# Kernel optimization log

Hardware: AMD Instinct MI355X
Metric: run time of the kernel (lower is better)

The kernel has to match this reference:

```python
import jax, jax.numpy as jnp
import numpy as np

D = 128          # hidden_dim
R = 16           # num_relations
N = 50000        # num_nodes
E = 800000       # num_edges
P = 256          # number of candidate paths
L = 4            # path length in nodes (max_path_length=3 edges)
NUM_LAYERS = 2


def _layer_norm(x, g, b, eps=1e-5):
    mu = jnp.mean(x, axis=-1, keepdims=True)
    var = jnp.var(x, axis=-1, keepdims=True)
    return (x - mu) * jax.lax.rsqrt(var + eps) * g + b


def _lstm(x, W_ih, W_hh, b):
    # x: (P, L, 2D) -> final hidden state (P, D). PyTorch gate order i,f,g,o.
    h0 = jnp.zeros((x.shape[0], D), x.dtype)
    c0 = jnp.zeros((x.shape[0], D), x.dtype)
    xs = jnp.swapaxes(x, 0, 1)  # (L, P, 2D)

    def step(carry, xt):
        h, c = carry
        gates = xt @ W_ih.T + h @ W_hh.T + b
        i, f, g, o = jnp.split(gates, 4, axis=-1)
        c = jax.nn.sigmoid(f) * c + jax.nn.sigmoid(i) * jnp.tanh(g)
        h = jax.nn.sigmoid(o) * jnp.tanh(c)
        return (h, c), None

    (h, _), _ = jax.lax.scan(step, (h0, c0), xs)
    return h


def setup_inputs() -> dict:
    key = jax.random.key(0)
    ks = jax.random.split(key, 24)
    s = 0.02
    inp = {
        'node_features': jax.random.normal(ks[0], (N, D), jnp.float32),
        'edge_index': jax.random.randint(ks[1], (2, E), 0, N),
        'edge_types': jax.random.randint(ks[2], (E,), 0, R),
        'query_embedding': jax.random.normal(ks[3], (D,), jnp.float32),
        'path_nodes': jax.random.randint(ks[4], (P, L), 0, N),
        'path_relations': jax.random.randint(ks[5], (P, L - 1), 0, R),
        # RGCN params (stacked over layers)
        'W_self': jax.random.normal(ks[6], (NUM_LAYERS, D, D), jnp.float32) * s,
        'b_self': jnp.zeros((NUM_LAYERS, D), jnp.float32),
        'W_rel': jax.random.normal(ks[7], (NUM_LAYERS, R, D, D), jnp.float32) * s,
        'ln_g': jnp.ones((NUM_LAYERS, D), jnp.float32),
        'ln_b': jnp.zeros((NUM_LAYERS, D), jnp.float32),
        # PathEncoder
        'rel_emb': jax.random.normal(ks[8], (R, D), jnp.float32) * s,
        'W_ih_f': jax.random.normal(ks[9], (4 * D, 2 * D), jnp.float32) * s,
        'W_hh_f': jax.random.normal(ks[10], (4 * D, D), jnp.float32) * s,
        'b_f': jnp.zeros((4 * D,), jnp.float32),
        'W_ih_b': jax.random.normal(ks[11], (4 * D, 2 * D), jnp.float32) * s,
        'W_hh_b': jax.random.normal(ks[12], (4 * D, D), jnp.float32) * s,
        'b_b': jnp.zeros((4 * D,), jnp.float32),
        'W_op': jax.random.normal(ks[13], (D, 2 * D), jnp.float32) * s,
        'b_op': jnp.zeros((D,), jnp.float32),
        # similarity scorer
        'W_s1': jax.random.normal(ks[14], (D, 2 * D), jnp.float32) * s,
        'b_s1': jnp.zeros((D,), jnp.float32),
        'W_s2': jax.random.normal(ks[15], (1, D), jnp.float32) * s,
        'b_s2': jnp.zeros((1,), jnp.float32),
    }
    return inp


def reference(node_features, edge_index, edge_types, query_embedding,
              path_nodes, path_relations,
              W_self, b_self, W_rel, ln_g, ln_b,
              rel_emb, W_ih_f, W_hh_f, b_f, W_ih_b, W_hh_b, b_b, W_op, b_op,
              W_s1, b_s1, W_s2, b_s2):
    src, dst = edge_index[0], edge_index[1]
    n = node_features.shape[0]
    deg = jnp.zeros((n,), node_features.dtype).at[dst].add(1.0)
    denom = jnp.maximum(deg, 1.0)[:, None]

    # ---- encode_subgraph: RGCN layers + LayerNorm ----
    x = node_features
    for l in range(NUM_LAYERS):
        trans = jnp.einsum('nd,rdk->rnk', x, W_rel[l])       # (R, N, D)
        msg = trans[edge_types, src]                          # (E, D) gather
        agg = jax.ops.segment_sum(msg, dst, num_segments=n) / denom
        x = jax.nn.relu(x @ W_self[l] + b_self[l] + agg)
        x = _layer_norm(x, ln_g[l], ln_b[l])
    encoded = x

    # ---- PathEncoder, batched over P paths ----
    pn = encoded[path_nodes]                                  # (P, L, D)
    rf = rel_emb[path_relations]                              # (P, L-1, D)
    zero_rel = jnp.zeros((rf.shape[0], 1, D), rf.dtype)
    rf = jnp.concatenate([zero_rel, rf], axis=1)              # (P, L, D)
    seq = jnp.concatenate([pn, rf], axis=-1)                  # (P, L, 2D)

    h_f = _lstm(seq, W_ih_f, W_hh_f, b_f)                     # forward final h
    h_b = _lstm(seq[:, ::-1, :], W_ih_b, W_hh_b, b_b)         # backward final h
    pe = jnp.concatenate([h_f, h_b], axis=-1)                 # (P, 2D)
    pe = jax.nn.relu(pe @ W_op.T + b_op)                      # (P, D)

    # ---- similarity scorer ----
    q = jnp.broadcast_to(query_embedding[None, :], pe.shape)
    comb = jnp.concatenate([pe, q], axis=-1)                  # (P, 2D)
    hdn = jax.nn.relu(comb @ W_s1.T + b_s1)
    sim = jax.nn.sigmoid(hdn @ W_s2.T + b_s2).squeeze(-1)     # (P,)

    return encoded, pe, sim
```

## Files before the change

kernel.cpp:

```cpp
#include <hip/hip_runtime.h>


#define NN 50000
#define EE 800000
#define DD 128
#define RR 16
#define PP 256
#define PADN 50048
#define NSLOT 17
#define CSTRIDE 136

typedef __attribute__((ext_vector_type(4))) float f32x4;
typedef __attribute__((ext_vector_type(2))) float f32x2;
typedef __attribute__((ext_vector_type(8))) short s16x8;

__device__ __forceinline__ float bf2f(unsigned int u16v){
    unsigned int u = u16v << 16;
    return __builtin_bit_cast(float, u);
}
__device__ __forceinline__ unsigned short f2bf(float f){
    unsigned int u = __builtin_bit_cast(unsigned int, f);
    u = u + 0x7fffu + ((u >> 16) & 1u);
    return (unsigned short)(u >> 16);
}

__global__ void k_hist(const int* __restrict__ dst, int* __restrict__ deg,
                       int* __restrict__ rank){
    int e = blockIdx.x*256 + threadIdx.x;
    if (e < EE) rank[e] = atomicAdd(&deg[dst[e]], 1);
}
__global__ void k_scan1(const int* __restrict__ deg, int* __restrict__ bsum){
    __shared__ int sm[256];
    int t = threadIdx.x, i = blockIdx.x*256 + t;
    sm[t] = (i < NN) ? deg[i] : 0;
    __syncthreads();
    for (int o = 128; o > 0; o >>= 1){
        if (t < o) sm[t] += sm[t+o];
        __syncthreads();
    }
    if (t == 0) bsum[blockIdx.x] = sm[0];
}
__global__ void k_scan2(const int* __restrict__ bsum, int* __restrict__ boff){
    __shared__ int sm[256];
    int t = threadIdx.x;
    int v = (t < 196) ? bsum[t] : 0;
    sm[t] = v;
    __syncthreads();
    for (int o = 1; o < 256; o <<= 1){
        int x = (t >= o) ? sm[t-o] : 0;
        __syncthreads();
        sm[t] += x;
        __syncthreads();
    }
    boff[t] = sm[t] - v;
}
__global__ void k_scan3(const int* __restrict__ deg, const int* __restrict__ boff,
                        int* __restrict__ row_start){
    __shared__ int sm[256];
    int t = threadIdx.x, i = blockIdx.x*256 + t;
    int v = (i < NN) ? deg[i] : 0;
    sm[t] = v;
    __syncthreads();
    for (int o = 1; o < 256; o <<= 1){
        int x = (t >= o) ? sm[t-o] : 0;
        __syncthreads();
        sm[t] += x;
        __syncthreads();
    }
    if (i < NN) row_start[i] = boff[blockIdx.x] + sm[t] - v;
    if (i == 0) row_start[NN] = EE;
}
__global__ void k_fill(const int* __restrict__ src, const int* __restrict__ dst,
                       const int* __restrict__ et, const int* __restrict__ row_start,
                       const int* __restrict__ rank, unsigned int* __restrict__ csr){
    int e = blockIdx.x*256 + threadIdx.x;
    if (e < EE){
        int pos = row_start[dst[e]] + rank[e];
        csr[pos] = ((unsigned int)et[e] << 16) | (unsigned int)src[e];
    }
}

__global__ void k_cvtx0(const float* __restrict__ nf, unsigned short* __restrict__ xb){
    int i = blockIdx.x*256 + threadIdx.x;
    if (i < PADN*DD) xb[i] = (i < NN*DD) ? f2bf(nf[i]) : (unsigned short)0;
}
__global__ void k_prep(const float* __restrict__ W_rel, const float* __restrict__ W_self,
                       const float* __restrict__ Wihf, const float* __restrict__ Wihb,
                       const float* __restrict__ Whhf, const float* __restrict__ Whhb,
                       const float* __restrict__ Wop,  const float* __restrict__ Ws1,
                       unsigned short* __restrict__ Bcat,
                       float* __restrict__ Wiht, float* __restrict__ Whht,
                       float* __restrict__ Wopt, float* __restrict__ Ws1t){
    int i = blockIdx.x*256 + threadIdx.x;
    if (i < 557056){
        int l  = i / (NSLOT*DD*DD);
        int r  = i % (NSLOT*DD*DD);
        int s  = r / (DD*DD);
        int r2 = r % (DD*DD);
        int ko = r2 / DD;
        int d  = r2 % DD;
        float v = (s < RR) ? W_rel[(((size_t)(l*RR + s))*DD + d)*DD + ko]
                           : W_self[((size_t)l*DD + d)*DD + ko];
        Bcat[i] = f2bf(v);
        return;
    }
    int i2 = i - 557056;
    if (i2 < 131072){ int j=i2/512, g=i2%512; Wiht[i2] = Wihf[g*256+j]; }
    else if (i2 < 262144){ int i3=i2-131072; int j=i3/512, g=i3%512; Wiht[131072+i3] = Wihb[g*256+j]; }
    else if (i2 < 327680){ int i3=i2-262144; int j=i3/512, g=i3%512; Whht[i3] = Whhf[g*128+j]; }
    else if (i2 < 393216){ int i3=i2-327680; int j=i3/512, g=i3%512; Whht[65536+i3] = Whhb[g*128+j]; }
    else if (i2 < 425984){ int i3=i2-393216; int j=i3/128, k=i3%128; Wopt[i3] = Wop[k*256+j]; }
    else if (i2 < 458752){ int i3=i2-425984; int j=i3/128, k=i3%128; Ws1t[i3] = Ws1[k*256+j]; }
}

__global__ __launch_bounds__(256, 2) void k_gemm(const unsigned short* __restrict__ A,
                                                 const unsigned short* __restrict__ Bt,
                                                 unsigned short* __restrict__ C)
{
    __shared__ unsigned short S[32768];
    unsigned short* As = S;
    unsigned short* Bs = S + 16384;
    const int m0 = blockIdx.x * 128;
    const int s  = blockIdx.y;
    const int tid  = threadIdx.x;
    const int wave = tid >> 6;
    const int lane = tid & 63;

    const unsigned short* gA = A + ((size_t)m0 + wave*32)*DD + lane*8;
    const unsigned short* gB = Bt + ((size_t)s*DD + wave*32)*DD + lane*8;
    unsigned short* lA = As + (wave*32)*DD;
    unsigned short* lB = Bs + (wave*32)*DD;
    for (int i = 0; i < 8; ++i){
        __builtin_amdgcn_global_load_lds((__attribute__((address_space(1))) const void*)(gA + i*512),
                                         (__attribute__((address_space(3))) void*)(lA + i*512), 16, 0, 0);
        __builtin_amdgcn_global_load_lds((__attribute__((address_space(1))) const void*)(gB + i*512),
                                         (__attribute__((address_space(3))) void*)(lB + i*512), 16, 0, 0);
    }
    __syncthreads();

    const int wm = wave & 1, wn = wave >> 1;
    f32x4 acc[4][4];
    for (int a=0;a<4;++a) for (int b=0;b<4;++b) acc[a][b] = (f32x4){0.f,0.f,0.f,0.f};

    for (int kb = 0; kb < 4; ++kb){
        const int koff = kb*32 + ((lane>>4)*8);
        s16x8 af[4], bfr[4];
        for (int mi=0;mi<4;++mi)
            af[mi] = *(const s16x8*)(As + (wm*64 + mi*16 + (lane&15))*DD + koff);
        for (int ni=0;ni<4;++ni)
            bfr[ni] = *(const s16x8*)(Bs + (wn*64 + ni*16 + (lane&15))*DD + koff);
        for (int mi=0;mi<4;++mi)
            for (int ni=0;ni<4;++ni)
                acc[mi][ni] = __builtin_amdgcn_mfma_f32_16x16x32_bf16(af[mi], bfr[ni], acc[mi][ni], 0, 0, 0);
    }
    __syncthreads();
    unsigned short* Cs = S;
    for (int mi=0;mi<4;++mi){
        int mrow0 = wm*64 + mi*16 + ((lane>>4)<<2);
        for (int ni=0;ni<4;++ni){
            int coln = wn*64 + ni*16 + (lane&15);
            for (int r=0;r<4;++r)
                Cs[(mrow0+r)*CSTRIDE + coln] = f2bf(acc[mi][ni][r]);
        }
    }
    __syncthreads();
    for (int ps = 0; ps < 8; ++ps){
        int idx = ps*256 + tid;
        int row = idx >> 4, seg = idx & 15;
        int m = m0 + row;
        if (m < NN)
            *(s16x8*)(C + ((size_t)s*NN + m)*DD + seg*8) = *(const s16x8*)(Cs + row*CSTRIDE + seg*8);
    }
}

__global__ __launch_bounds__(256) void k_aggfin(
    const unsigned short* __restrict__ transc, const unsigned int* __restrict__ csr,
    const int* __restrict__ row_start, const unsigned short* __restrict__ selfT,
    const float* __restrict__ bs, const float* __restrict__ lg, const float* __restrict__ lb,
    float* __restrict__ xf, unsigned short* __restrict__ xb, int write_f)
{
    int nd = blockIdx.x*4 + (threadIdx.x >> 6);
    int lane = threadIdx.x & 63;
    if (nd >= NN){
        if (!write_f && nd < PADN) ((unsigned int*)xb)[(size_t)nd*64 + lane] = 0u;
        return;
    }
    int rs = row_start[nd], re = row_start[nd+1];
    float a0 = 0.f, a1 = 0.f;
    int e = rs;
    for (; e + 2 <= re; e += 2){
        unsigned int v1 = csr[e], v2 = csr[e+1];
        unsigned int pv1 = *((const unsigned int*)(transc +
            ((size_t)(v1 >> 16)*NN + (v1 & 0xffffu))*DD) + lane);
        unsigned int pv2 = *((const unsigned int*)(transc +
            ((size_t)(v2 >> 16)*NN + (v2 & 0xffffu))*DD) + lane);
        a0 += bf2f(pv1 & 0xffffu) + bf2f(pv2 & 0xffffu);
        a1 += bf2f(pv1 >> 16)     + bf2f(pv2 >> 16);
    }
    if (e < re){
        unsigned int v1 = csr[e];
        unsigned int pv1 = *((const unsigned int*)(transc +
            ((size_t)(v1 >> 16)*NN + (v1 & 0xffffu))*DD) + lane);
        a0 += bf2f(pv1 & 0xffffu);
        a1 += bf2f(pv1 >> 16);
    }
    float dn = fmaxf((float)(re - rs), 1.f);
    unsigned int sv = ((const unsigned int*)selfT)[(size_t)nd*64 + lane];
    float y0 = bf2f(sv & 0xffffu) + bs[lane*2]   + a0/dn;
    float y1 = bf2f(sv >> 16)     + bs[lane*2+1] + a1/dn;
    y0 = fmaxf(y0, 0.f); y1 = fmaxf(y1, 0.f);
    float s1 = y0 + y1, s2 = y0*y0 + y1*y1;
    for (int off = 32; off > 0; off >>= 1){
        s1 += __shfl_xor(s1, off);
        s2 += __shfl_xor(s2, off);
    }
    float mu  = s1 * (1.f/128.f);
    float var = s2 * (1.f/128.f) - mu*mu;
    float inv = rsqrtf(var + 1e-5f);
    float o0 = (y0 - mu)*inv*lg[lane*2]   + lb[lane*2];
    float o1 = (y1 - mu)*inv*lg[lane*2+1] + lb[lane*2+1];
    if (write_f)
        *(f32x2*)(xf + (size_t)nd*DD + lane*2) = (f32x2){o0, o1};
    else
        ((unsigned int*)xb)[(size_t)nd*64 + lane] =
            (unsigned int)f2bf(o0) | ((unsigned int)f2bf(o1) << 16);
}

__global__ __launch_bounds__(256) void k_gin(const float* __restrict__ enc,
                                             const int* __restrict__ pn,
                                             const int* __restrict__ pr,
                                             const float* __restrict__ rel_emb,
                                             const float* __restrict__ Wiht,
                                             float* __restrict__ gi){
    int b = blockIdx.x;
    int dir = b >> 7;
    int blk = b & 127;
    int pairs0 = blk * 8;
    int tid = threadIdx.x;
    int group = tid >> 7;
    int tl = tid & 127;
    __shared__ float sq[8][256];
    for (int k = 0; k < 2; ++k){
        int idx = tid + 256*k;
        int row = idx >> 6;
        int off = (idx & 63) * 4;
        int pair = pairs0 + row;
        int p = pair >> 2, tt = pair & 3;
        int tsel = dir ? (3 - tt) : tt;
        f32x4 v;
        if (off < 128){
            int node = pn[p*4 + tsel];
            v = *(const f32x4*)&enc[(size_t)node*DD + off];
        } else if (tsel == 0){
            v = (f32x4){0.f,0.f,0.f,0.f};
        } else {
            int rel = pr[p*3 + (tsel-1)];
            v = *(const f32x4*)&rel_emb[(size_t)rel*DD + (off-128)];
        }
        *(f32x4*)&sq[row][off] = v;
    }
    __syncthreads();
    const float* W = Wiht + (size_t)dir*131072;
    float acc[4][4];
    for (int a=0;a<4;++a) for (int g=0;g<4;++g) acc[a][g]=0.f;
    for (int j4 = 0; j4 < 256; j4 += 4){
        f32x4 sv[4];
        for (int q=0;q<4;++q) sv[q] = *(const f32x4*)&sq[group*4+q][j4];
        for (int jj = 0; jj < 4; ++jj){
            int j = j4 + jj;
            float w0 = W[(size_t)j*512 + tl];
            float w1 = W[(size_t)j*512 + tl + 128];
            float w2 = W[(size_t)j*512 + tl + 256];
            float w3 = W[(size_t)j*512 + tl + 384];
            for (int q=0;q<4;++q){
                float sval = sv[q][jj];
                acc[q][0] += sval*w0;
                acc[q][1] += sval*w1;
                acc[q][2] += sval*w2;
                acc[q][3] += sval*w3;
            }
        }
    }
    for (int q=0;q<4;++q){
        int pair = pairs0 + group*4 + q;
        float* dstp = gi + ((size_t)dir*1024 + pair)*512;
        dstp[tl]     = acc[q][0];
        dstp[tl+128] = acc[q][1];
        dstp[tl+256] = acc[q][2];
        dstp[tl+384] = acc[q][3];
    }
}
__global__ __launch_bounds__(256) void k_rec(const float* __restrict__ gi,
                                             const float* __restrict__ Whht,
                                             const float* __restrict__ b_f,
                                             const float* __restrict__ b_b,
                                             float* __restrict__ hbuf){
    int b = blockIdx.x;
    int dir = b >> 6;
    int pg = b & 63;
    int p0 = pg * 4;
    int tid = threadIdx.x;
    int group = tid >> 7;
    int tl = tid & 127;
    __shared__ float hs[4][128], cs[4][128], gb[4][512];
    {
        int it = tid;       hs[it>>7][it&127] = 0.f; cs[it>>7][it&127] = 0.f;
        it = tid + 256;     hs[it>>7][it&127] = 0.f; cs[it>>7][it&127] = 0.f;
    }
    __syncthreads();
    const float* W = Whht + (size_t)dir*65536;
    const float* bias = dir ? b_b : b_f;
    float bb0 = bias[tl], bb1 = bias[tl+128], bb2 = bias[tl+256], bb3 = bias[tl+384];
    for (int t = 0; t < 4; ++t){
        float acc[2][4];
        for (int pl = 0; pl < 2; ++pl){
            int p = p0 + group*2 + pl;
            const float* gp = gi + ((size_t)dir*1024 + p*4 + t)*512;
            acc[pl][0] = gp[tl]     + bb0;
            acc[pl][1] = gp[tl+128] + bb1;
            acc[pl][2] = gp[tl+256] + bb2;
            acc[pl][3] = gp[tl+384] + bb3;
        }
        for (int j4 = 0; j4 < 128; j4 += 4){
            f32x4 hv0 = *(const f32x4*)&hs[group*2][j4];
            f32x4 hv1 = *(const f32x4*)&hs[group*2+1][j4];
            for (int jj = 0; jj < 4; ++jj){
                int j = j4 + jj;
                float w0 = W[(size_t)j*512 + tl];
                float w1 = W[(size_t)j*512 + tl + 128];
                float w2 = W[(size_t)j*512 + tl + 256];
                float w3 = W[(size_t)j*512 + tl + 384];
                float h0 = hv0[jj], h1 = hv1[jj];
                acc[0][0] += h0*w0; acc[0][1] += h0*w1; acc[0][2] += h0*w2; acc[0][3] += h0*w3;
                acc[1][0] += h1*w0; acc[1][1] += h1*w1; acc[1][2] += h1*w2; acc[1][3] += h1*w3;
            }
        }
        for (int pl = 0; pl < 2; ++pl){
            int pidx = group*2 + pl;
            gb[pidx][tl]     = acc[pl][0];
            gb[pidx][tl+128] = acc[pl][1];
            gb[pidx][tl+256] = acc[pl][2];
            gb[pidx][tl+384] = acc[pl][3];
        }
        __syncthreads();
        for (int r = 0; r < 2; ++r){
            int it = tid + 256*r;
            int pidx = it >> 7, k = it & 127;
            float giv = gb[pidx][k], gfv = gb[pidx][128+k], ggv = gb[pidx][256+k], gov = gb[pidx][384+k];
            float si = 1.f/(1.f + expf(-giv));
            float sf = 1.f/(1.f + expf(-gfv));
            float so = 1.f/(1.f + expf(-gov));
            float cn = sf*cs[pidx][k] + si*tanhf(ggv);
            cs[pidx][k] = cn;
            hs[pidx][k] = so*tanhf(cn);
        }
        __syncthreads();
    }
    for (int r = 0; r < 2; ++r){
        int it = tid + 256*r;
        int pidx = it >> 7, k = it & 127;
        hbuf[((size_t)dir*PP + p0 + pidx)*DD + k] = hs[pidx][k];
    }
}
__global__ __launch_bounds__(256) void k_head(const float* __restrict__ hbuf,
    const float* __restrict__ query, const float* __restrict__ Wopt, const float* __restrict__ Ws1t,
    const float* __restrict__ b_op, const float* __restrict__ b_s1,
    const float* __restrict__ W_s2, const float* __restrict__ b_s2,
    float* __restrict__ out)
{
    int pb = blockIdx.x * 8;
    int tid = threadIdx.x;
    __shared__ float cat[8][256];
    __shared__ float pe_l[8][128];
    __shared__ float hd_l[8][128];
    __shared__ float qs[128];
    __shared__ float part[8][2];
    for (int k = 0; k < 8; ++k){
        int i = tid + 256*k;
        int p = i >> 8, j = i & 255;
        float v = (j < 128) ? hbuf[(size_t)(pb+p)*DD + j]
                            : hbuf[(size_t)(PP + pb + p)*DD + (j-128)];
        cat[p][j] = v;
    }
    if (tid < 128) qs[tid] = query[tid];
    __syncthreads();
    int k = tid & 127;
    int sub = tid >> 7;
    for (int r = 0; r < 4; ++r){
        int p = sub + 2*r;
        float a = b_op[k];
        for (int j = 0; j < 256; ++j) a += Wopt[j*128 + k] * cat[p][j];
        a = fmaxf(a, 0.f);
        pe_l[p][k] = a;
        out[(size_t)NN*DD + (size_t)(pb+p)*DD + k] = a;
    }
    __syncthreads();
    for (int r = 0; r < 4; ++r){
        int p = sub + 2*r;
        float a = b_s1[k];
        for (int j = 0; j < 128; ++j) a += Ws1t[j*128 + k] * pe_l[p][j];
        for (int j = 0; j < 128; ++j) a += Ws1t[(128+j)*128 + k] * qs[j];
        hd_l[p][k] = fmaxf(a, 0.f);
    }
    __syncthreads();
    for (int r = 0; r < 4; ++r){
        int p = sub + 2*r;
        float v = W_s2[k] * hd_l[p][k];
        for (int off = 32; off > 0; off >>= 1) v += __shfl_xor(v, off);
        if ((tid & 63) == 0) part[p][(tid>>6)&1] = v;
    }
    __syncthreads();
    if (tid < 8){
        float sv = part[tid][0] + part[tid][1] + b_s2[0];
        out[(size_t)NN*DD + (size_t)PP*DD + pb + tid] = 1.f/(1.f + expf(-sv));
    }
}

extern "C" void kernel_launch(void* const* d_in, const int* in_sizes, int n_in,
                              void* d_out, int out_size, void* d_ws, size_t ws_size,
                              hipStream_t stream)
{
    (void)in_sizes; (void)n_in; (void)out_size; (void)ws_size;
    const float* nf      = (const float*)d_in[0];
    const int*   ei      = (const int*)d_in[1];
    const int*   et      = (const int*)d_in[2];
    const float* query   = (const float*)d_in[3];
    const int*   pn      = (const int*)d_in[4];
    const int*   pr      = (const int*)d_in[5];
    const float* W_self  = (const float*)d_in[6];
    const float* b_self  = (const float*)d_in[7];
    const float* W_rel   = (const float*)d_in[8];
    const float* ln_g    = (const float*)d_in[9];
    const float* ln_b    = (const float*)d_in[10];
    const float* rel_emb = (const float*)d_in[11];
    const float* W_ih_f  = (const float*)d_in[12];
    const float* W_hh_f  = (const float*)d_in[13];
    const float* b_f     = (const float*)d_in[14];
    const float* W_ih_b  = (const float*)d_in[15];
    const float* W_hh_b  = (const float*)d_in[16];
    const float* b_b     = (const float*)d_in[17];
    const float* W_op    = (const float*)d_in[18];
    const float* b_op    = (const float*)d_in[19];
    const float* W_s1    = (const float*)d_in[20];
    const float* b_s1    = (const float*)d_in[21];
    const float* W_s2    = (const float*)d_in[22];
    const float* b_s2    = (const float*)d_in[23];
    float* out = (float*)d_out;

    char* wp = (char*)d_ws;
    size_t off = 0;
    auto alloc = [&](size_t bytes)->void*{
        void* p = wp + off;
        off += (bytes + 255) & ~(size_t)255;
        return p;
    };
    int* deg        = (int*)alloc((size_t)NN*4);
    int* row_start  = (int*)alloc((size_t)(NN+1)*4);
    int* rank       = (int*)alloc((size_t)EE*4);
    int* bsum       = (int*)alloc(256*4);
    int* boff       = (int*)alloc(256*4);
    unsigned int* csr = (unsigned int*)alloc((size_t)EE*4);
    unsigned short* x0b   = (unsigned short*)alloc((size_t)PADN*DD*2);
    unsigned short* x1b   = (unsigned short*)alloc((size_t)PADN*DD*2);
    unsigned short* selfT = (unsigned short*)alloc((size_t)NN*DD*2);
    unsigned short* Bcat  = (unsigned short*)alloc((size_t)2*NSLOT*DD*DD*2);
    float* Wiht = (float*)alloc((size_t)262144*4);
    float* Whht = (float*)alloc((size_t)131072*4);
    float* Wopt = (float*)alloc((size_t)32768*4);
    float* Ws1t = (float*)alloc((size_t)32768*4);
    float* gi   = (float*)alloc((size_t)2*1024*512*4);
    float* hbuf = (float*)alloc((size_t)2*PP*DD*4);
    unsigned short* trans = (unsigned short*)alloc((size_t)16*NN*DD*2);

    hipMemsetAsync(deg, 0, (size_t)NN*4, stream);
    k_hist<<<(EE+255)/256, 256, 0, stream>>>(ei + EE, deg, rank);
    k_scan1<<<196, 256, 0, stream>>>(deg, bsum);
    k_scan2<<<1, 256, 0, stream>>>(bsum, boff);
    k_scan3<<<196, 256, 0, stream>>>(deg, boff, row_start);
    k_fill<<<(EE+255)/256, 256, 0, stream>>>(ei, ei + EE, et, row_start, rank, csr);
    k_cvtx0<<<(PADN*DD+255)/256, 256, 0, stream>>>(nf, x0b);
    k_prep<<<3968, 256, 0, stream>>>(W_rel, W_self, W_ih_f, W_ih_b, W_hh_f, W_hh_b, W_op, W_s1,
                                     Bcat, Wiht, Whht, Wopt, Ws1t);
    for (int l = 0; l < 2; ++l){
        const unsigned short* xin = l ? x1b : x0b;
        const unsigned short* Bl  = Bcat + (size_t)l*NSLOT*DD*DD;
        k_gemm<<<dim3(PADN/128, 16), 256, 0, stream>>>(xin, Bl, trans);
        k_gemm<<<dim3(PADN/128, 1), 256, 0, stream>>>(xin, Bl + (size_t)16*DD*DD, selfT);
        if (l == 0)
            k_aggfin<<<PADN/4, 256, 0, stream>>>(trans, csr, row_start, selfT,
                b_self, ln_g, ln_b, nullptr, x1b, 0);
        else
            k_aggfin<<<PADN/4, 256, 0, stream>>>(trans, csr, row_start, selfT,
                b_self + DD, ln_g + DD, ln_b + DD, out, nullptr, 1);
    }
    k_gin<<<256, 256, 0, stream>>>(out, pn, pr, rel_emb, Wiht, gi);
    k_rec<<<128, 256, 0, stream>>>(gi, Whht, b_f, b_b, hbuf);
    k_head<<<32, 256, 0, stream>>>(hbuf, query, Wopt, Ws1t, b_op, b_s1, W_s2, b_s2, out);
}
```

Before: 601.1 us.

## Swizzle bf16 GEMM operands for LDS, fuse prep kernels, merge self GEMM slot

Operand matrices (node features, layer-1 activations and weight blocks) are now stored in global memory with an XOR swizzle of 8-element chunks keyed by row. The GEMM reads LDS with the matching swizzled column, which is meant to remove LDS bank conflicts on the MFMA fragment loads. The fill, conversion and weight-prep kernels are merged into one launch. The self-weight GEMM now runs as a 17th slot of the main GEMM grid writing into an enlarged trans buffer, which removes a separate launch and buffer. The cost is a more complex indexing scheme that must stay consistent across producers and the consumer.

Measured after the change: 532.9 us. 1.13x faster.

```diff
diff --git a/kernel.cpp b/kernel.cpp
--- a/kernel.cpp
+++ b/kernel.cpp
@@ -70,35 +70,45 @@
     if (i < NN) row_start[i] = boff[blockIdx.x] + sm[t] - v;
     if (i == 0) row_start[NN] = EE;
 }
-__global__ void k_fill(const int* __restrict__ src, const int* __restrict__ dst,
-                       const int* __restrict__ et, const int* __restrict__ row_start,
-                       const int* __restrict__ rank, unsigned int* __restrict__ csr){
-    int e = blockIdx.x*256 + threadIdx.x;
-    if (e < EE){
+
+#define NB_FILL 3125
+#define NB_CVT  25024
+#define NB_PREP 3968
+__global__ void k_fused(const int* __restrict__ src, const int* __restrict__ dst,
+                        const int* __restrict__ et, const int* __restrict__ row_start,
+                        const int* __restrict__ rank, unsigned int* __restrict__ csr,
+                        const float* __restrict__ nf, unsigned short* __restrict__ xb,
+                        const float* __restrict__ W_rel, const float* __restrict__ W_self,
+                        const float* __restrict__ Wihf, const float* __restrict__ Wihb,
+                        const float* __restrict__ Whhf, const float* __restrict__ Whhb,
+                        const float* __restrict__ Wop,  const float* __restrict__ Ws1,
+                        unsigned short* __restrict__ Bcat,
+                        float* __restrict__ Wiht, float* __restrict__ Whht,
+                        float* __restrict__ Wopt, float* __restrict__ Ws1t){
+    int b = blockIdx.x;
+    if (b < NB_FILL){
+        int e = b*256 + threadIdx.x;
         int pos = row_start[dst[e]] + rank[e];
         csr[pos] = ((unsigned int)et[e] << 16) | (unsigned int)src[e];
-    }
-}
-
-__global__ void k_cvtx0(const float* __restrict__ nf, unsigned short* __restrict__ xb){
-    int i = blockIdx.x*256 + threadIdx.x;
-    if (i < PADN*DD) xb[i] = (i < NN*DD) ? f2bf(nf[i]) : (unsigned short)0;
-}
-__global__ void k_prep(const float* __restrict__ W_rel, const float* __restrict__ W_self,
-                       const float* __restrict__ Wihf, const float* __restrict__ Wihb,
-                       const float* __restrict__ Whhf, const float* __restrict__ Whhb,
-                       const float* __restrict__ Wop,  const float* __restrict__ Ws1,
-                       unsigned short* __restrict__ Bcat,
-                       float* __restrict__ Wiht, float* __restrict__ Whht,
-                       float* __restrict__ Wopt, float* __restrict__ Ws1t){
-    int i = blockIdx.x*256 + threadIdx.x;
+        return;
+    }
+    if (b < NB_FILL + NB_CVT){
+        int i = (b - NB_FILL)*256 + threadIdx.x;
+        int r  = i >> 7;
+        int dd = i & 127;
+        int d  = (((dd >> 3) ^ (r & 15)) << 3) | (dd & 7);
+        xb[i] = (r < NN) ? f2bf(nf[(size_t)r*DD + d]) : (unsigned short)0;
+        return;
+    }
+    int i = (b - NB_FILL - NB_CVT)*256 + threadIdx.x;
     if (i < 557056){
         int l  = i / (NSLOT*DD*DD);
         int r  = i % (NSLOT*DD*DD);
         int s  = r / (DD*DD);
         int r2 = r % (DD*DD);
         int ko = r2 / DD;
-        int d  = r2 % DD;
+        int dd = r2 % DD;
+        int d  = (((dd >> 3) ^ (ko & 15)) << 3) | (dd & 7);
         float v = (s < RR) ? W_rel[(((size_t)(l*RR + s))*DD + d)*DD + ko]
                            : W_self[((size_t)l*DD + d)*DD + ko];
         Bcat[i] = f2bf(v);
@@ -143,12 +153,12 @@
     for (int a=0;a<4;++a) for (int b=0;b<4;++b) acc[a][b] = (f32x4){0.f,0.f,0.f,0.f};
 
     for (int kb = 0; kb < 4; ++kb){
-        const int koff = kb*32 + ((lane>>4)*8);
+        const int cx = (((kb << 2) + (lane >> 4)) ^ (lane & 15)) << 3;
         s16x8 af[4], bfr[4];
         for (int mi=0;mi<4;++mi)
-            af[mi] = *(const s16x8*)(As + (wm*64 + mi*16 + (lane&15))*DD + koff);
+            af[mi] = *(const s16x8*)(As + (wm*64 + mi*16 + (lane&15))*DD + cx);
         for (int ni=0;ni<4;++ni)
-            bfr[ni] = *(const s16x8*)(Bs + (wn*64 + ni*16 + (lane&15))*DD + koff);
+            bfr[ni] = *(const s16x8*)(Bs + (wn*64 + ni*16 + (lane&15))*DD + cx);
         for (int mi=0;mi<4;++mi)
             for (int ni=0;ni<4;++ni)
                 acc[mi][ni] = __builtin_amdgcn_mfma_f32_16x16x32_bf16(af[mi], bfr[ni], acc[mi][ni], 0, 0, 0);
@@ -174,8 +184,8 @@
 }
 
 __global__ __launch_bounds__(256) void k_aggfin(
-    const unsigned short* __restrict__ transc, const unsigned int* __restrict__ csr,
-    const int* __restrict__ row_start, const unsigned short* __restrict__ selfT,
+    const unsigned short* __restrict__ trans, const unsigned int* __restrict__ csr,
+    const int* __restrict__ row_start,
     const float* __restrict__ bs, const float* __restrict__ lg, const float* __restrict__ lb,
     float* __restrict__ xf, unsigned short* __restrict__ xb, int write_f)
 {
@@ -190,22 +200,22 @@
     int e = rs;
     for (; e + 2 <= re; e += 2){
         unsigned int v1 = csr[e], v2 = csr[e+1];
-        unsigned int pv1 = *((const unsigned int*)(transc +
+        unsigned int pv1 = *((const unsigned int*)(trans +
             ((size_t)(v1 >> 16)*NN + (v1 & 0xffffu))*DD) + lane);
-        unsigned int pv2 = *((const unsigned int*)(transc +
+        unsigned int pv2 = *((const unsigned int*)(trans +
             ((size_t)(v2 >> 16)*NN + (v2 & 0xffffu))*DD) + lane);
         a0 += bf2f(pv1 & 0xffffu) + bf2f(pv2 & 0xffffu);
         a1 += bf2f(pv1 >> 16)     + bf2f(pv2 >> 16);
     }
     if (e < re){
         unsigned int v1 = csr[e];
-        unsigned int pv1 = *((const unsigned int*)(transc +
+        unsigned int pv1 = *((const unsigned int*)(trans +
             ((size_t)(v1 >> 16)*NN + (v1 & 0xffffu))*DD) + lane);
         a0 += bf2f(pv1 & 0xffffu);
         a1 += bf2f(pv1 >> 16);
     }
     float dn = fmaxf((float)(re - rs), 1.f);
-    unsigned int sv = ((const unsigned int*)selfT)[(size_t)nd*64 + lane];
+    unsigned int sv = ((const unsigned int*)trans)[(size_t)16*NN*64 + (size_t)nd*64 + lane];
     float y0 = bf2f(sv & 0xffffu) + bs[lane*2]   + a0/dn;
     float y1 = bf2f(sv >> 16)     + bs[lane*2+1] + a1/dn;
     y0 = fmaxf(y0, 0.f); y1 = fmaxf(y1, 0.f);
@@ -221,9 +231,11 @@
     float o1 = (y1 - mu)*inv*lg[lane*2+1] + lb[lane*2+1];
     if (write_f)
         *(f32x2*)(xf + (size_t)nd*DD + lane*2) = (f32x2){o0, o1};
-    else
-        ((unsigned int*)xb)[(size_t)nd*64 + lane] =
+    else {
+        int sw = (((lane >> 2) ^ (nd & 15)) << 2) | (lane & 3);
+        ((unsigned int*)xb)[(size_t)nd*64 + sw] =
             (unsigned int)f2bf(o0) | ((unsigned int)f2bf(o1) << 16);
+    }
 }
 
 __global__ __launch_bounds__(256) void k_gin(const float* __restrict__ enc,
@@ -462,7 +474,6 @@
     unsigned int* csr = (unsigned int*)alloc((size_t)EE*4);
     unsigned short* x0b   = (unsigned short*)alloc((size_t)PADN*DD*2);
     unsigned short* x1b   = (unsigned short*)alloc((size_t)PADN*DD*2);
-    unsigned short* selfT = (unsigned short*)alloc((size_t)NN*DD*2);
     unsigned short* Bcat  = (unsigned short*)alloc((size_t)2*NSLOT*DD*DD*2);
     float* Wiht = (float*)alloc((size_t)262144*4);
     float* Whht = (float*)alloc((size_t)131072*4);
@@ -470,27 +481,26 @@
     float* Ws1t = (float*)alloc((size_t)32768*4);
     float* gi   = (float*)alloc((size_t)2*1024*512*4);
     float* hbuf = (float*)alloc((size_t)2*PP*DD*4);
-    unsigned short* trans = (unsigned short*)alloc((size_t)16*NN*DD*2);
+    unsigned short* trans = (unsigned short*)alloc((size_t)NSLOT*NN*DD*2);
 
     hipMemsetAsync(deg, 0, (size_t)NN*4, stream);
     k_hist<<<(EE+255)/256, 256, 0, stream>>>(ei + EE, deg, rank);
     k_scan1<<<196, 256, 0, stream>>>(deg, bsum);
     k_scan2<<<1, 256, 0, stream>>>(bsum, boff);
     k_scan3<<<196, 256, 0, stream>>>(deg, boff, row_start);
-    k_fill<<<(EE+255)/256, 256, 0, stream>>>(ei, ei + EE, et, row_start, rank, csr);
-    k_cvtx0<<<(PADN*DD+255)/256, 256, 0, stream>>>(nf, x0b);
-    k_prep<<<3968, 256, 0, stream>>>(W_rel, W_self, W_ih_f, W_ih_b, W_hh_f, W_hh_b, W_op, W_s1,
-                                     Bcat, Wiht, Whht, Wopt, Ws1t);
+    k_fused<<<NB_FILL + NB_CVT + NB_PREP, 256, 0, stream>>>(
+        ei, ei + EE, et, row_start, rank, csr, nf, x0b,
+        W_rel, W_self, W_ih_f, W_ih_b, W_hh_f, W_hh_b, W_op, W_s1,
+        Bcat, Wiht, Whht, Wopt, Ws1t);
     for (int l = 0; l < 2; ++l){
         const unsigned short* xin = l ? x1b : x0b;
         const unsigned short* Bl  = Bcat + (size_t)l*NSLOT*DD*DD;
-        k_gemm<<<dim3(PADN/128, 16), 256, 0, stream>>>(xin, Bl, trans);
-        k_gemm<<<dim3(PADN/128, 1), 256, 0, stream>>>(xin, Bl + (size_t)16*DD*DD, selfT);
+        k_gemm<<<dim3(PADN/128, NSLOT), 256, 0, stream>>>(xin, Bl, trans);
         if (l == 0)
-            k_aggfin<<<PADN/4, 256, 0, stream>>>(trans, csr, row_start, selfT,
+            k_aggfin<<<PADN/4, 256, 0, stream>>>(trans, csr, row_start,
                 b_self, ln_g, ln_b, nullptr, x1b, 0);
         else
-            k_aggfin<<<PADN/4, 256, 0, stream>>>(trans, csr, row_start, selfT,
+            k_aggfin<<<PADN/4, 256, 0, stream>>>(trans, csr, row_start,
                 b_self + DD, ln_g + DD, ln_b + DD, out, nullptr, 1);
     }
     k_gin<<<256, 256, 0, stream>>>(out, pn, pr, rel_emb, Wiht, gi);
```
